# Kernel optimization log

Measured on AMD Instinct MI355X. Metric: run time of the kernel, lower is better.

Reference implementation:

```python
import jax, jax.numpy as jnp
import numpy as np
import math

B, T, M, C, H = 2, 2048, 1024, 512, 8
D = C // H  # head dim = 64


def setup_inputs() -> dict:
    key = jax.random.key(0)
    ks = jax.random.split(key, 6)
    return {
        "x": jax.random.normal(ks[0], (B, T, C), jnp.float32),
        "y": jax.random.normal(ks[1], (B, M, C), jnp.float32),
        "attn_x_mask": jnp.ones((1, 1, T, T), jnp.int32),
        "qkv_w": jax.random.normal(ks[2], (3 * C, C), jnp.float32) * 0.02,
        "qkv_b": jax.random.normal(ks[3], (3 * C,), jnp.float32) * 0.02,
        "proj_w": jax.random.normal(ks[4], (C, C), jnp.float32) * 0.02,
        "proj_b": jax.random.normal(ks[5], (C,), jnp.float32) * 0.02,
    }


def _split_heads(t, n, d):
    # [B, N, C] -> [B, H, N, D]
    b = t.shape[0]
    return t.reshape(b, n, H, d).transpose(0, 2, 1, 3)


def reference(x, y, attn_x_mask, qkv_w, qkv_b, proj_w, proj_b):
    b, t, c = x.shape
    m = y.shape[1]
    d = c // H
    scale = 1.0 / math.sqrt(d)

    # shared qkv projection applied to x and y (torch Linear: x @ W.T + b)
    qkv_x = x @ qkv_w.T + qkv_b
    q_x, k_x, v_x = jnp.split(qkv_x, 3, axis=-1)
    qkv_y = y @ qkv_w.T + qkv_b
    q_y, k_y, v_y = jnp.split(qkv_y, 3, axis=-1)

    q_x, k_x, v_x = (_split_heads(a, t, d) for a in (q_x, k_x, v_x))
    q_y, k_y, v_y = (_split_heads(a, m, d) for a in (q_y, k_y, v_y))

    # x -> y cross attention scores (pre-softmax, reused for chaining)
    catt_x2y = jnp.einsum("bhtd,bhmd->bhtm", q_x, k_y) * scale  # [B,H,T,M]
    cval_x2y = jnp.einsum("bhtm,bhmd->bhtd", jax.nn.softmax(catt_x2y, axis=-1), v_y)
    cval_x2y = cval_x2y.transpose(0, 2, 1, 3).reshape(b, t, c)

    # y -> x scores, then chained through raw x2y scores
    catt_y2x = jnp.einsum("bhmd,bhsd->bhms", q_y, k_x) * scale  # [B,H,M,T]
    chained = jnp.einsum("bhtm,bhms->bhts", catt_x2y, catt_y2x) * scale  # [B,H,T,T]
    chained = jnp.where(attn_x_mask == 0, -jnp.inf, chained)
    cval_y2x = jnp.einsum("bhts,bhsd->bhtd", jax.nn.softmax(chained, axis=-1), v_x)
    cval_y2x = cval_y2x.transpose(0, 2, 1, 3).reshape(b, t, c)

    out = cval_x2y - cval_y2x
    out = out @ proj_w.T + proj_b  # dropout layers are identity in eval mode
    return out
```

## Files before the change

kernel.cpp:

```cpp
#include <hip/hip_runtime.h>


typedef _Float16 half_t;
typedef _Float16 half8 __attribute__((ext_vector_type(8)));
typedef _Float16 half4v __attribute__((ext_vector_type(4)));
typedef float floatx4 __attribute__((ext_vector_type(4)));
typedef int int4v __attribute__((ext_vector_type(4)));

constexpr int Bc = 2, Tc = 2048, Mc = 1024, Cc = 512, Hc = 8, Dc = 64;
constexpr long BTC = (long)Bc * Tc * Cc;
constexpr long ZT  = (long)Bc * Hc * Tc;
constexpr float S1 = 0.18033688f;

enum { EPI_F16STORE = 0, EPI_QKV_XY = 1, EPI_PROJ = 2 };

struct EpiParams {
  half_t* h0;
  half_t* h1;
  half_t* h2;
  half_t* h3;
  half_t* h4;
  half_t* h5;
  half_t* h6;
  float* f0;
  const float* bias;
  float scale;
  int ldc;
  long bstride;
};

__device__ __forceinline__ void gld_lds16(const half_t* g, half_t* l) {
  __builtin_amdgcn_global_load_lds(
      (const __attribute__((address_space(1))) void*)g,
      (__attribute__((address_space(3))) void*)l, 16, 0, 0);
}

__device__ __forceinline__ int pkrtz(float a, float b) {
  return __builtin_bit_cast(int, __builtin_amdgcn_cvt_pkrtz(a, b));
}
__device__ __forceinline__ void pl16(int& a, int& b) {
  asm volatile("v_permlane16_swap_b32 %0, %1" : "+v"(a), "+v"(b));
}
__device__ __forceinline__ void pl32(int& a, int& b) {
  asm volatile("v_permlane32_swap_b32 %0, %1" : "+v"(a), "+v"(b));
}

template <int BM, int BN, int WMG, int WNG, int EPI, int GX = 0, int GY = 0>
__global__ __launch_bounds__(256) void gemm_nt(
    const half_t* __restrict__ A, const half_t* __restrict__ Bt,
    int K, int lda, int ldb, long bsA, long bsB, EpiParams ep)
{
  constexpr int BK = 64;
  constexpr int WTM = BM / WMG, WTN = BN / WNG;
  constexpr int MI = WTM / 16, NI = WTN / 16;
  constexpr int AIT = BM * BK / 8 / 256;
  constexpr int BIT = BN * BK / 8 / 256;
  constexpr int NLD = AIT + BIT;
  __shared__ __align__(16) half_t As[2][BM * BK];
  __shared__ __align__(16) half_t Bs[2][BN * BK];

  const int tid = threadIdx.x;
  const int lane = tid & 63;
  const int wave = tid >> 6;
  const int wm = wave / WNG, wn = wave % WNG;
  const int r16 = lane & 15, g = lane >> 4;
  const int z = blockIdx.z;

  int bxl = blockIdx.x, byl = blockIdx.y;
  if constexpr (GX > 0) {
    constexpr int CHUNK = GX * GY / 8;
    const int f = byl * GX + bxl;
    const int L = (f & 7) * CHUNK + (f >> 3);
    bxl = L % GX; byl = L / GX;
  }
  const long m0 = (long)byl * BM;
  const long n0 = (long)bxl * BN;
  const half_t* Abase = A + (long)z * bsA + m0 * (long)lda;
  const half_t* Bbase = Bt + (long)z * bsB + n0 * (long)ldb;

  const int rA = wm * WTM + r16;
  const int rB = wn * WTN + r16;

  floatx4 acc[MI][NI];
#pragma unroll
  for (int mi = 0; mi < MI; ++mi)
#pragma unroll
    for (int ni = 0; ni < NI; ++ni)
      acc[mi][ni] = floatx4{0.f, 0.f, 0.f, 0.f};

  auto stage = [&](int kt, int buf) {
#pragma unroll
    for (int i = 0; i < AIT; ++i) {
      const int c = tid + i * 256;
      const int row = c >> 3, js = c & 7;
      const int jg = js ^ (row & 7);
      gld_lds16(Abase + (long)row * lda + kt + jg * 8, &As[buf][c * 8]);
    }
#pragma unroll
    for (int i = 0; i < BIT; ++i) {
      const int c = tid + i * 256;
      const int row = c >> 3, js = c & 7;
      const int jg = js ^ (row & 7);
      gld_lds16(Bbase + (long)row * ldb + kt + jg * 8, &Bs[buf][c * 8]);
    }
  };

  const int NIT = K / BK;
  stage(0, 0);
  asm volatile("" ::: "memory");

  for (int it = 0; it < NIT; ++it) {
    const bool hn = (it + 1 < NIT);
    if (hn) stage((it + 1) * BK, (it + 1) & 1);
    asm volatile("" ::: "memory");
    if (hn) {
      if constexpr (NLD == 6) asm volatile("s_waitcnt vmcnt(6)" ::: "memory");
      else if constexpr (NLD == 4) asm volatile("s_waitcnt vmcnt(4)" ::: "memory");
      else if constexpr (NLD == 8) asm volatile("s_waitcnt vmcnt(8)" ::: "memory");
      else asm volatile("s_waitcnt vmcnt(0)" ::: "memory");
    } else {
      asm volatile("s_waitcnt vmcnt(0)" ::: "memory");
    }
    __builtin_amdgcn_s_barrier();
    asm volatile("" ::: "memory");

    const half_t* Ab = As[it & 1];
    const half_t* Bb = Bs[it & 1];
    half8 aF[MI][2], bF[NI][2];
#pragma unroll
    for (int mi = 0; mi < MI; ++mi)
#pragma unroll
      for (int k2 = 0; k2 < 2; ++k2)
        aF[mi][k2] = *reinterpret_cast<const half8*>(
            &Ab[(rA + mi * 16) * BK + ((k2 * 4 + g) ^ (r16 & 7)) * 8]);
#pragma unroll
    for (int ni = 0; ni < NI; ++ni)
#pragma unroll
      for (int k2 = 0; k2 < 2; ++k2)
        bF[ni][k2] = *reinterpret_cast<const half8*>(
            &Bb[(rB + ni * 16) * BK + ((k2 * 4 + g) ^ (r16 & 7)) * 8]);
    __builtin_amdgcn_s_setprio(1);
#pragma unroll
    for (int k2 = 0; k2 < 2; ++k2)
#pragma unroll
      for (int mi = 0; mi < MI; ++mi)
#pragma unroll
        for (int ni = 0; ni < NI; ++ni)
          acc[mi][ni] = __builtin_amdgcn_mfma_f32_16x16x32_f16(
              aF[mi][k2], bF[ni][k2], acc[mi][ni], 0, 0, 0);
    __builtin_amdgcn_s_setprio(0);
    asm volatile("s_waitcnt lgkmcnt(0)" ::: "memory");
    __builtin_amdgcn_s_barrier();
    asm volatile("" ::: "memory");
  }

  half_t* Txp = &As[0][0];
  const bool isx  = (m0 < (long)Bc * Tc);
  const int which = (int)(n0 >> 9);
  const int hh    = ((int)n0 & 511) >> 6;

#pragma unroll
  for (int mi = 0; mi < MI; ++mi) {
#pragma unroll
    for (int ni = 0; ni < NI; ++ni) {
#pragma unroll
      for (int reg = 0; reg < 4; ++reg) {
        const int r = (int)m0 + wm * WTM + mi * 16 + g * 4 + reg;
        const int c = (int)n0 + wn * WTN + ni * 16 + r16;
        const float v = acc[mi][ni][reg];
        if constexpr (EPI == EPI_F16STORE) {
          ep.h0[(long)z * ep.bstride + (long)r * ep.ldc + c] = (half_t)(v * ep.scale);
        } else if constexpr (EPI == EPI_QKV_XY) {
          const float val = v + ep.bias[c];
          const int d = c & 63;
          const int rloc = r - (int)m0;
          if (isx) {
            const int b = (int)(m0 >> 11);
            const int t = r & (Tc - 1);
            const long bh = (long)(b * Hc + hh);
            if (which == 0)      ep.h0[(bh * Tc + t) * Dc + d] = (half_t)(val * S1);
            else if (which == 1) ep.h1[(bh * Tc + t) * Dc + d] = (half_t)val;
            else                 Txp[d * 136 + rloc] = (half_t)val;
          } else {
            const long m2 = m0 - (long)Bc * Tc;
            const int b = (int)(m2 >> 10);
            const int t = (r - Bc * Tc) & (Mc - 1);
            const long bh = (long)(b * Hc + hh);
            if (which == 0)      Txp[d * 136 + rloc] = (half_t)(val * 0.125f);
            else if (which == 1) { ep.h4[(bh * Mc + t) * Dc + d] = (half_t)val;
                                   Txp[d * 136 + rloc] = (half_t)val; }
            else                 Txp[d * 136 + rloc] = (half_t)val;
          }
        } else {
          ep.f0[(long)r * Cc + c] = v + ep.bias[c];
        }
      }
    }
  }

  if constexpr (EPI == EPI_QKV_XY && BM == 128) {
    const bool hasT = isx ? (which == 2) : true;
    if (hasT) {
      __syncthreads();
      half_t* dstT; int L; long tb; int b;
      if (isx) { dstT = ep.h2; L = Tc; tb = m0 & (Tc - 1); b = (int)(m0 >> 11); }
      else {
        const long m2 = m0 - (long)Bc * Tc;
        b = (int)(m2 >> 10); tb = m2 & (Mc - 1); L = Mc;
        dstT = (which == 0) ? ep.h3 : (which == 1) ? ep.h5 : ep.h6;
      }
      const long bh = (long)(b * Hc + hh);
      const int dr = tid >> 2, qd = tid & 3;
      half_t* gbase = dstT + (bh * 64 + dr) * L + tb + qd * 32;
#pragma unroll
      for (int j = 0; j < 4; ++j) {
        const half8 v8 = *reinterpret_cast<const half8*>(&Txp[dr * 136 + qd * 32 + j * 8]);
        *reinterpret_cast<half8*>(&gbase[j * 8]) = v8;
      }
    }
  }
}

__global__ __launch_bounds__(256) void wtq2(
    const half_t* __restrict__ QYT, const half_t* __restrict__ KYT,
    const half_t* __restrict__ QX, half_t* __restrict__ Q2)
{
  __shared__ __align__(16) half_t As[2][4096];
  __shared__ __align__(16) half_t Bs[2][4096];
  __shared__ __align__(16) half_t WTs[4096];
  const int tid = threadIdx.x, lane = tid & 63, wave = tid >> 6;
  const int wm = wave >> 1, wn = wave & 1;
  const int r16 = lane & 15, g = lane >> 4;
  const int f = blockIdx.x;
  const int L = (f & 7) * 32 + (f >> 3);
  const int z = L >> 4;
  const int t0 = (L & 15) * 128;
  const half_t* Aq = QYT + (long)z * Dc * Mc;
  const half_t* Bk = KYT + (long)z * Dc * Mc;

  auto stage1 = [&](int kt, int buf) {
#pragma unroll
    for (int i = 0; i < 2; ++i) {
      const int c = tid + i * 256;
      const int row = c >> 3, js = c & 7, jg = js ^ (row & 7);
      gld_lds16(Aq + (long)row * Mc + kt + jg * 8, &As[buf][c * 8]);
    }
#pragma unroll
    for (int i = 0; i < 2; ++i) {
      const int c = tid + i * 256;
      const int row = c >> 3, js = c & 7, jg = js ^ (row & 7);
      gld_lds16(Bk + (long)row * Mc + kt + jg * 8, &Bs[buf][c * 8]);
    }
  };

  floatx4 acc[2][2];
#pragma unroll
  for (int mi = 0; mi < 2; ++mi)
#pragma unroll
    for (int ni = 0; ni < 2; ++ni) acc[mi][ni] = floatx4{0.f, 0.f, 0.f, 0.f};

  const int rA = wm * 32 + r16, rB = wn * 32 + r16;
  stage1(0, 0);
  asm volatile("" ::: "memory");
  for (int it = 0; it < 16; ++it) {
    const bool hn = (it < 15);
    if (hn) stage1((it + 1) * 64, (it + 1) & 1);
    asm volatile("" ::: "memory");
    if (hn) asm volatile("s_waitcnt vmcnt(4)" ::: "memory");
    else    asm volatile("s_waitcnt vmcnt(0)" ::: "memory");
    __builtin_amdgcn_s_barrier();
    asm volatile("" ::: "memory");
    const half_t* Ab = As[it & 1];
    const half_t* Bb = Bs[it & 1];
    half8 aF[2][2], bF[2][2];
#pragma unroll
    for (int mi = 0; mi < 2; ++mi)
#pragma unroll
      for (int k2 = 0; k2 < 2; ++k2)
        aF[mi][k2] = *reinterpret_cast<const half8*>(
            &Ab[(rA + mi * 16) * 64 + ((k2 * 4 + g) ^ (r16 & 7)) * 8]);
#pragma unroll
    for (int ni = 0; ni < 2; ++ni)
#pragma unroll
      for (int k2 = 0; k2 < 2; ++k2)
        bF[ni][k2] = *reinterpret_cast<const half8*>(
            &Bb[(rB + ni * 16) * 64 + ((k2 * 4 + g) ^ (r16 & 7)) * 8]);
    __builtin_amdgcn_s_setprio(1);
#pragma unroll
    for (int k2 = 0; k2 < 2; ++k2)
#pragma unroll
      for (int mi = 0; mi < 2; ++mi)
#pragma unroll
        for (int ni = 0; ni < 2; ++ni)
          acc[mi][ni] = __builtin_amdgcn_mfma_f32_16x16x32_f16(
              aF[mi][k2], bF[ni][k2], acc[mi][ni], 0, 0, 0);
    __builtin_amdgcn_s_setprio(0);
    asm volatile("s_waitcnt lgkmcnt(0)" ::: "memory");
    __builtin_amdgcn_s_barrier();
    asm volatile("" ::: "memory");
  }

  half_t* P2 = &As[0][0];
#pragma unroll
  for (int i = 0; i < 4; ++i) {
    const int c = tid + i * 256;
    const int row = c >> 3, js = c & 7, jg = js ^ (row & 7);
    gld_lds16(QX + ((long)z * Tc + t0 + row) * 64 + jg * 8, P2 + c * 8);
  }
#pragma unroll
  for (int mi = 0; mi < 2; ++mi)
#pragma unroll
    for (int ni = 0; ni < 2; ++ni)
#pragma unroll
      for (int reg = 0; reg < 4; ++reg) {
        const int r = wm * 32 + mi * 16 + g * 4 + reg;
        const int c = wn * 32 + ni * 16 + r16;
        WTs[r * 64 + (((c >> 3) ^ (r & 7)) << 3) + (c & 7)] =
            (half_t)(acc[mi][ni][reg] * 0.125f);
      }
  __syncthreads();

  floatx4 a2[2][4];
#pragma unroll
  for (int mi = 0; mi < 2; ++mi)
#pragma unroll
    for (int ni = 0; ni < 4; ++ni) a2[mi][ni] = floatx4{0.f, 0.f, 0.f, 0.f};
  const int rA2 = wave * 32 + r16;
  half8 aF2[2][2], bF2[4][2];
#pragma unroll
  for (int mi = 0; mi < 2; ++mi)
#pragma unroll
    for (int k2 = 0; k2 < 2; ++k2)
      aF2[mi][k2] = *reinterpret_cast<const half8*>(
          &P2[(rA2 + mi * 16) * 64 + ((k2 * 4 + g) ^ (r16 & 7)) * 8]);
#pragma unroll
  for (int ni = 0; ni < 4; ++ni)
#pragma unroll
    for (int k2 = 0; k2 < 2; ++k2)
      bF2[ni][k2] = *reinterpret_cast<const half8*>(
          &WTs[(ni * 16 + r16) * 64 + ((k2 * 4 + g) ^ (r16 & 7)) * 8]);
#pragma unroll
  for (int k2 = 0; k2 < 2; ++k2)
#pragma unroll
    for (int mi = 0; mi < 2; ++mi)
#pragma unroll
      for (int ni = 0; ni < 4; ++ni)
        a2[mi][ni] = __builtin_amdgcn_mfma_f32_16x16x32_f16(
            aF2[mi][k2], bF2[ni][k2], a2[mi][ni], 0, 0, 0);
#pragma unroll
  for (int mi = 0; mi < 2; ++mi)
#pragma unroll
    for (int ni = 0; ni < 4; ++ni)
#pragma unroll
      for (int reg = 0; reg < 4; ++reg) {
        const int t = t0 + wave * 32 + mi * 16 + g * 4 + reg;
        const int c = ni * 16 + r16;
        Q2[((long)z * Tc + t) * 64 + c] = (half_t)a2[mi][ni][reg];
      }
}

__device__ __forceinline__ void stageK128(const half_t* Kz, int s0, half_t* dst, int tid) {
#pragma unroll
  for (int i = 0; i < 4; ++i) {
    const int c = tid + i * 256;
    const int row = c >> 3, js = c & 7;
    const int jg = js ^ (row & 7);
    gld_lds16(Kz + (long)(s0 + row) * 64 + jg * 8, dst + c * 8);
  }
}
__device__ __forceinline__ void stageV128(const half_t* Vz, int s0, int Slen, half_t* dst, int tid) {
#pragma unroll
  for (int i = 0; i < 4; ++i) {
    const int c = tid + i * 256;
    const int row = c >> 4, js = c & 15;
    const int jg = js ^ (row & 15);
    gld_lds16(Vz + (long)row * Slen + s0 + jg * 8, dst + c * 8);
  }
}

template <bool MASKED, bool PARTIAL>
__device__ __forceinline__ void flash_body(
    const half_t* __restrict__ Qp, const half_t* __restrict__ Kp,
    const half_t* __restrict__ Vp, const unsigned char* __restrict__ mpk,
    half_t* __restrict__ POh, float* __restrict__ Lp, half_t* __restrict__ outF,
    int Slen, int sbeg, int scount, int z, int q0,
    half_t* Kb0, half_t* Kb1, half_t* Vb)
{
  const int tid = threadIdx.x, lane = tid & 63, w = tid >> 6;
  const int r16 = lane & 15, g = lane >> 4;
  const int b = z >> 3, h = z & 7;
  const int NT = Slen >> 7;
  const half_t* Qz = Qp + ((long)z * Tc + q0) * 64;
  const half_t* Kz = Kp + (long)z * Slen * 64;
  const half_t* Vz = Vp + (long)z * 64 * Slen;

  stageK128(Kz, sbeg, Kb0, tid);
  asm volatile("" ::: "memory");
  stageV128(Vz, sbeg, Slen, Vb, tid);
  asm volatile("" ::: "memory");

  half8 aQ[2][2];
#pragma unroll
  for (int mi = 0; mi < 2; ++mi)
#pragma unroll
    for (int k2 = 0; k2 < 2; ++k2)
      aQ[mi][k2] = *reinterpret_cast<const half8*>(
          Qz + (w * 32 + mi * 16 + r16) * 64 + k2 * 32 + g * 8);

  half8 vones;
#pragma unroll
  for (int j = 0; j < 8; ++j) vones[j] = (half_t)1.f;

  floatx4 oaccT[2][4];
  floatx4 lacc4[2];
#pragma unroll
  for (int mi = 0; mi < 2; ++mi) {
    lacc4[mi] = floatx4{0.f, 0.f, 0.f, 0.f};
#pragma unroll
    for (int no = 0; no < 4; ++no) oaccT[mi][no] = floatx4{0.f, 0.f, 0.f, 0.f};
  }

  const int send = sbeg + scount;
  int cur = 0;
  for (int s0 = sbeg; s0 < send; s0 += 128) {
    const bool hn = (s0 + 128 < send);
    asm volatile("s_waitcnt vmcnt(4)" ::: "memory");
    __builtin_amdgcn_s_barrier();
    asm volatile("" ::: "memory");

    unsigned int mb32[2];
    if constexpr (MASKED) {
      const int tile = s0 >> 7;
#pragma unroll
      for (int mi = 0; mi < 2; ++mi) {
        const int q = q0 + w * 32 + mi * 16 + r16;
        mb32[mi] = *reinterpret_cast<const unsigned int*>(
            mpk + ((long)q * NT + tile) * 16 + 4 * g);
      }
    }

    floatx4 sacc[2][8];
#pragma unroll
    for (int mi = 0; mi < 2; ++mi)
#pragma unroll
      for (int ni = 0; ni < 8; ++ni) sacc[mi][ni] = floatx4{0.f, 0.f, 0.f, 0.f};
    const half_t* Kc = cur ? Kb1 : Kb0;
    __builtin_amdgcn_s_setprio(1);
#pragma unroll
    for (int ni = 0; ni < 8; ++ni) {
      const int rB = ni * 16 + r16;
      const half8 b0 = *reinterpret_cast<const half8*>(&Kc[rB * 64 + (g ^ (rB & 7)) * 8]);
      const half8 b1 = *reinterpret_cast<const half8*>(&Kc[rB * 64 + ((4 + g) ^ (rB & 7)) * 8]);
#pragma unroll
      for (int mi = 0; mi < 2; ++mi) {
        sacc[mi][ni] = __builtin_amdgcn_mfma_f32_16x16x32_f16(b0, aQ[mi][0], sacc[mi][ni], 0, 0, 0);
        sacc[mi][ni] = __builtin_amdgcn_mfma_f32_16x16x32_f16(b1, aQ[mi][1], sacc[mi][ni], 0, 0, 0);
      }
    }
    __builtin_amdgcn_s_setprio(0);
    if (hn) stageK128(Kz, s0 + 128, cur ? Kb0 : Kb1, tid);
    asm volatile("" ::: "memory");

#pragma unroll
    for (int mi = 0; mi < 2; ++mi) {
      if constexpr (MASKED) {
        if (mb32[mi] != 0xffffffffu) {
#pragma unroll
          for (int reg = 0; reg < 4; ++reg)
#pragma unroll
            for (int ni = 0; ni < 8; ++ni)
              if (!((mb32[mi] >> (reg * 8 + ni)) & 1)) sacc[mi][ni][reg] = -__builtin_inff();
        }
      }
#pragma unroll
      for (int ni = 0; ni < 8; ++ni)
#pragma unroll
        for (int reg = 0; reg < 4; ++reg)
          sacc[mi][ni][reg] = __builtin_amdgcn_exp2f(sacc[mi][ni][reg]);
    }

    if (hn) { asm volatile("s_waitcnt vmcnt(4)" ::: "memory"); }
    else    { asm volatile("s_waitcnt vmcnt(0)" ::: "memory"); }
    __builtin_amdgcn_s_barrier();
    asm volatile("" ::: "memory");

#pragma unroll
    for (int c = 0; c < 4; ++c) {
      half8 bVv[4];
#pragma unroll
      for (int no = 0; no < 4; ++no) {
        const int rV = no * 16 + r16;
        bVv[no] = *reinterpret_cast<const half8*>(
            &Vb[rV * 128 + ((c * 4 + g) ^ (rV & 15)) * 8]);
      }
#pragma unroll
      for (int mi = 0; mi < 2; ++mi) {
        int x0 = pkrtz(sacc[mi][2 * c][0],     sacc[mi][2 * c][1]);
        int x1 = pkrtz(sacc[mi][2 * c][2],     sacc[mi][2 * c][3]);
        int x2 = pkrtz(sacc[mi][2 * c + 1][0], sacc[mi][2 * c + 1][1]);
        int x3 = pkrtz(sacc[mi][2 * c + 1][2], sacc[mi][2 * c + 1][3]);
        pl32(x0, x2); pl32(x1, x3);
        pl16(x0, x2); pl16(x1, x3);
        int4v wv; wv[0] = x0; wv[1] = x1; wv[2] = x2; wv[3] = x3;
        const half8 aP = __builtin_bit_cast(half8, wv);
        __builtin_amdgcn_s_setprio(1);
#pragma unroll
        for (int no = 0; no < 4; ++no)
          oaccT[mi][no] = __builtin_amdgcn_mfma_f32_16x16x32_f16(bVv[no], aP, oaccT[mi][no], 0, 0, 0);
        lacc4[mi] = __builtin_amdgcn_mfma_f32_16x16x32_f16(vones, aP, lacc4[mi], 0, 0, 0);
        __builtin_amdgcn_s_setprio(0);
      }
    }
    __builtin_amdgcn_s_barrier();
    asm volatile("" ::: "memory");
    if (hn) stageV128(Vz, s0 + 128, Slen, Vb, tid);
    asm volatile("" ::: "memory");
    cur ^= 1;
  }

  float ls2[2];
#pragma unroll
  for (int mi = 0; mi < 2; ++mi) ls2[mi] = lacc4[mi][0];

  float* slab = reinterpret_cast<float*>(Vb) + w * 1024;
#pragma unroll
  for (int mi = 0; mi < 2; ++mi) {
    const int tq = q0 + w * 32 + mi * 16;
    if constexpr (PARTIAL) {
      if (lane < 16) Lp[(long)z * Tc + tq + r16] = ls2[mi];
    }
    const float sc = PARTIAL ? 1.f : (1.f / ls2[mi]);
#pragma unroll
    for (int no = 0; no < 4; ++no) {
      floatx4 v = oaccT[mi][no];
      if constexpr (!PARTIAL) v *= sc;
      *reinterpret_cast<floatx4*>(&slab[r16 * 64 + no * 16 + (g ^ (r16 & 3)) * 4]) = v;
    }
#pragma unroll
    for (int it = 0; it < 4; ++it) {
      const int q2 = it * 4 + g;
      const int d4 = r16;
      const floatx4 v = *reinterpret_cast<const floatx4*>(
          &slab[q2 * 64 + (d4 >> 2) * 16 + ((d4 & 3) ^ (q2 & 3)) * 4]);
      const long off = ((long)(b * Tc + tq + q2)) * Cc + h * 64 + d4 * 4;
      half4v hh; hh[0] = (half_t)v[0]; hh[1] = (half_t)v[1];
      hh[2] = (half_t)v[2]; hh[3] = (half_t)v[3];
      if constexpr (PARTIAL) {
        *reinterpret_cast<half4v*>(&POh[off]) = hh;
      } else {
        *reinterpret_cast<half4v*>(&outF[off]) = hh;
      }
    }
  }
}

__global__ __launch_bounds__(256, 3) void flash_both(
    const half_t* __restrict__ Q2, const half_t* __restrict__ KX,
    const half_t* __restrict__ VXT, const unsigned char* __restrict__ mpk,
    const half_t* __restrict__ QX, const half_t* __restrict__ KY,
    const half_t* __restrict__ VYT,
    half_t* __restrict__ POh, float* __restrict__ Lp, half_t* __restrict__ DH2)
{
  __shared__ __align__(16) half_t Kb0[8192];
  __shared__ __align__(16) half_t Kb1[8192];
  __shared__ __align__(16) half_t Vb[8192];
  const int bx = blockIdx.x;
  if (bx < 512) {
    const int z  = ((bx & 7) << 1) | ((bx >> 3) & 1);
    const int sh = (bx >> 4) & 1;
    const int q0 = (bx >> 5) * 128;
    flash_body<true, true>(Q2, KX, VXT, mpk,
                           POh + (long)sh * BTC, Lp + (long)sh * ZT, nullptr,
                           Tc, sh * 1024, 1024, z, q0, Kb0, Kb1, Vb);
  } else {
    const int b2 = bx - 512;
    const int z  = ((b2 & 7) << 1) | ((b2 >> 3) & 1);
    const int q0 = (b2 >> 4) * 128;
    flash_body<false, false>(QX, KY, VYT, nullptr,
                             nullptr, nullptr, DH2,
                             Mc, 0, Mc, z, q0, Kb0, Kb1, Vb);
  }
}

__global__ __launch_bounds__(256) void combine_k(
    const half_t* __restrict__ POh, const float* __restrict__ Lp,
    const half_t* __restrict__ DH2, half_t* __restrict__ DH)
{
  const long idx = (long)blockIdx.x * 256 + threadIdx.x;
  const long c4 = idx * 4;
  const int c = (int)(c4 & (Cc - 1));
  const long bt = c4 >> 9;
  const int h = c >> 6;
  const int b = (int)(bt >> 11), t = (int)(bt & (Tc - 1));
  const long zt = (long)(b * Hc + h) * Tc + t;
  const float ainv = 1.f / (Lp[zt] + Lp[ZT + zt]);
  const half4v oa0 = reinterpret_cast<const half4v*>(POh)[idx];
  const half4v oa1 = reinterpret_cast<const half4v*>(POh)[BTC / 4 + idx];
  const half4v dv = reinterpret_cast<const half4v*>(DH2)[idx];
  half4v r;
  r[0] = (half_t)((float)dv[0] - ((float)oa0[0] + (float)oa1[0]) * ainv);
  r[1] = (half_t)((float)dv[1] - ((float)oa0[1] + (float)oa1[1]) * ainv);
  r[2] = (half_t)((float)dv[2] - ((float)oa0[2] + (float)oa1[2]) * ainv);
  r[3] = (half_t)((float)dv[3] - ((float)oa0[3] + (float)oa1[3]) * ainv);
  reinterpret_cast<half4v*>(DH)[idx] = r;
}

__device__ __forceinline__ void cvt4(const float* in, half_t* out, long i) {
  const float4 f = reinterpret_cast<const float4*>(in)[i];
  half4v h; h[0] = (half_t)f.x; h[1] = (half_t)f.y; h[2] = (half_t)f.z; h[3] = (half_t)f.w;
  reinterpret_cast<half4v*>(out)[i] = h;
}

__global__ __launch_bounds__(256) void prep(
    const float* __restrict__ x, const float* __restrict__ y,
    const float* __restrict__ qw, const float* __restrict__ pw,
    const int* __restrict__ mask,
    half_t* __restrict__ XH, half_t* __restrict__ YH,
    half_t* __restrict__ WQ, half_t* __restrict__ WP,
    unsigned char* __restrict__ mpk)
{
  const long i = (long)blockIdx.x * 256 + threadIdx.x;
  constexpr long n0 = 524288;
  constexpr long n1 = n0 + 262144;
  constexpr long n2 = n1 + 196608;
  constexpr long n3 = n2 + 65536;
  if (i < n0) cvt4(x, XH, i);
  else if (i < n1) cvt4(y, YH, i - n0);
  else if (i < n2) cvt4(qw, WQ, i - n1);
  else if (i < n3) cvt4(pw, WP, i - n2);
  else {
    const long idx = i - n3;
    const int t = (int)(idx >> 8), tile = (int)((idx >> 4) & 15), r16 = (int)(idx & 15);
    const int* row = mask + (long)t * Tc + tile * 128 + r16;
    unsigned int bbits = 0;
#pragma unroll
    for (int ni = 0; ni < 8; ++ni)
      bbits |= (row[ni * 16] != 0 ? 1u : 0u) << ni;
    mpk[idx] = (unsigned char)bbits;
  }
}

constexpr size_t OFF_XH   = 0;
constexpr size_t OFF_YH   = OFF_XH   + (size_t)Bc*Tc*Cc*2;
constexpr size_t OFF_WQ   = OFF_YH   + (size_t)Bc*Mc*Cc*2;
constexpr size_t OFF_WP   = OFF_WQ   + (size_t)3*Cc*Cc*2;
constexpr size_t OFF_QX   = OFF_WP   + (size_t)Cc*Cc*2;
constexpr size_t OFF_KX   = OFF_QX   + (size_t)Bc*Hc*Tc*Dc*2;
constexpr size_t OFF_VXT  = OFF_KX   + (size_t)Bc*Hc*Tc*Dc*2;
constexpr size_t OFF_QYT  = OFF_VXT  + (size_t)Bc*Hc*Tc*Dc*2;
constexpr size_t OFF_KY   = OFF_QYT  + (size_t)Bc*Hc*Mc*Dc*2;
constexpr size_t OFF_KYT  = OFF_KY   + (size_t)Bc*Hc*Mc*Dc*2;
constexpr size_t OFF_VYT  = OFF_KYT  + (size_t)Bc*Hc*Mc*Dc*2;
constexpr size_t OFF_Q2   = OFF_VYT  + (size_t)Bc*Hc*Mc*Dc*2;
constexpr size_t OFF_DH   = OFF_Q2   + (size_t)Bc*Hc*Tc*Dc*2;
constexpr size_t OFF_DH2  = OFF_DH   + (size_t)Bc*Tc*Cc*2;
constexpr size_t OFF_MPK  = OFF_DH2  + (size_t)Bc*Tc*Cc*2;
constexpr size_t OFF_PO   = OFF_MPK  + (size_t)Tc*256;
constexpr size_t OFF_L    = OFF_PO   + (size_t)2*BTC*2;

extern "C" void kernel_launch(void* const* d_in, const int* in_sizes, int n_in,
                              void* d_out, int out_size, void* d_ws, size_t ws_size,
                              hipStream_t stream) {
  const float* x      = (const float*)d_in[0];
  const float* y      = (const float*)d_in[1];
  const int*   mask   = (const int*)  d_in[2];
  const float* qkv_b  = (const float*)d_in[4];
  const float* proj_b = (const float*)d_in[6];
  float* out = (float*)d_out;
  char* ws = (char*)d_ws;

  half_t* XH   = (half_t*)(ws + OFF_XH);
  half_t* YH   = (half_t*)(ws + OFF_YH);
  half_t* WQ   = (half_t*)(ws + OFF_WQ);
  half_t* WP   = (half_t*)(ws + OFF_WP);
  half_t* QX   = (half_t*)(ws + OFF_QX);
  half_t* KX   = (half_t*)(ws + OFF_KX);
  half_t* VXT  = (half_t*)(ws + OFF_VXT);
  half_t* QYT  = (half_t*)(ws + OFF_QYT);
  half_t* KY   = (half_t*)(ws + OFF_KY);
  half_t* KYT  = (half_t*)(ws + OFF_KYT);
  half_t* VYT  = (half_t*)(ws + OFF_VYT);
  half_t* Q2   = (half_t*)(ws + OFF_Q2);
  half_t* DH   = (half_t*)(ws + OFF_DH);
  half_t* DH2  = (half_t*)(ws + OFF_DH2);
  unsigned char* MPK = (unsigned char*)(ws + OFF_MPK);
  half_t* POh  = (half_t*)(ws + OFF_PO);
  float*  Lp   = (float*) (ws + OFF_L);

  prep<<<6144, 256, 0, stream>>>(x, y, (const float*)d_in[3], (const float*)d_in[5],
                                 mask, XH, YH, WQ, WP, MPK);

  {
    EpiParams ep{};
    ep.h0 = QX; ep.h1 = KX; ep.h2 = VXT; ep.h3 = QYT;
    ep.h4 = KY; ep.h5 = KYT; ep.h6 = VYT; ep.bias = qkv_b;
    gemm_nt<128,64,2,2,EPI_QKV_XY,24,48><<<dim3(24, 48, 1), 256, 0, stream>>>(
        XH, WQ, Cc, Cc, Cc, 0, 0, ep);
  }

  wtq2<<<dim3(256), 256, 0, stream>>>(QYT, KYT, QX, Q2);

  flash_both<<<dim3(768), 256, 0, stream>>>(
      Q2, KX, VXT, MPK, QX, KY, VYT, POh, Lp, DH2);

  combine_k<<<(int)(BTC/4/256), 256, 0, stream>>>(POh, Lp, DH2, DH);

  {
    EpiParams ep{}; ep.f0 = out; ep.bias = proj_b;
    gemm_nt<64,64,2,2,EPI_PROJ,8,64><<<dim3(8, 64, 1), 256, 0, stream>>>(
        DH, WP, Cc, Cc, Cc, 0, 0, ep);
  }
}
```

Baseline: 173.5 us.

## Split flash attention into finer KV chunks with 64-wide tiles and six-way combine

```diff
diff --git a/kernel.cpp b/kernel.cpp
--- a/kernel.cpp
+++ b/kernel.cpp
@@ -359,32 +359,31 @@
       }
 }
 
-__device__ __forceinline__ void stageK128(const half_t* Kz, int s0, half_t* dst, int tid) {
-#pragma unroll
-  for (int i = 0; i < 4; ++i) {
+__device__ __forceinline__ void stageK64(const half_t* Kz, int s0, half_t* dst, int tid) {
+#pragma unroll
+  for (int i = 0; i < 2; ++i) {
     const int c = tid + i * 256;
     const int row = c >> 3, js = c & 7;
     const int jg = js ^ (row & 7);
     gld_lds16(Kz + (long)(s0 + row) * 64 + jg * 8, dst + c * 8);
   }
 }
-__device__ __forceinline__ void stageV128(const half_t* Vz, int s0, int Slen, half_t* dst, int tid) {
-#pragma unroll
-  for (int i = 0; i < 4; ++i) {
+__device__ __forceinline__ void stageV64(const half_t* Vz, int s0, int Slen, half_t* dst, int tid) {
+#pragma unroll
+  for (int i = 0; i < 2; ++i) {
     const int c = tid + i * 256;
-    const int row = c >> 4, js = c & 15;
-    const int jg = js ^ (row & 15);
+    const int row = c >> 3, js = c & 7;
+    const int jg = js ^ (row & 7);
     gld_lds16(Vz + (long)row * Slen + s0 + jg * 8, dst + c * 8);
   }
 }
 
-template <bool MASKED, bool PARTIAL>
+template <bool MASKED>
 __device__ __forceinline__ void flash_body(
     const half_t* __restrict__ Qp, const half_t* __restrict__ Kp,
     const half_t* __restrict__ Vp, const unsigned char* __restrict__ mpk,
-    half_t* __restrict__ POh, float* __restrict__ Lp, half_t* __restrict__ outF,
-    int Slen, int sbeg, int scount, int z, int q0,
-    half_t* Kb0, half_t* Kb1, half_t* Vb)
+    half_t* __restrict__ POh, float* __restrict__ Lp,
+    int Slen, int sbeg, int z, int q0, half_t* lds)
 {
   const int tid = threadIdx.x, lane = tid & 63, w = tid >> 6;
   const int r16 = lane & 15, g = lane >> 4;
@@ -393,10 +392,13 @@
   const half_t* Qz = Qp + ((long)z * Tc + q0) * 64;
   const half_t* Kz = Kp + (long)z * Slen * 64;
   const half_t* Vz = Vp + (long)z * 64 * Slen;
-
-  stageK128(Kz, sbeg, Kb0, tid);
+  half_t* Kb0 = lds;
+  half_t* Kb1 = lds + 4096;
+  half_t* Vb  = lds + 8192;
+
+  stageK64(Kz, sbeg, Kb0, tid);
   asm volatile("" ::: "memory");
-  stageV128(Vz, sbeg, Slen, Vb, tid);
+  stageV64(Vz, sbeg, Slen, Vb, tid);
   asm volatile("" ::: "memory");
 
   half8 aQ[2][2];
@@ -420,11 +422,11 @@
     for (int no = 0; no < 4; ++no) oaccT[mi][no] = floatx4{0.f, 0.f, 0.f, 0.f};
   }
 
-  const int send = sbeg + scount;
+  const int send = sbeg + 512;
   int cur = 0;
-  for (int s0 = sbeg; s0 < send; s0 += 128) {
-    const bool hn = (s0 + 128 < send);
-    asm volatile("s_waitcnt vmcnt(4)" ::: "memory");
+  for (int s0 = sbeg; s0 < send; s0 += 64) {
+    const bool hn = (s0 + 64 < send);
+    asm volatile("s_waitcnt vmcnt(2)" ::: "memory");
     __builtin_amdgcn_s_barrier();
     asm volatile("" ::: "memory");
 
@@ -438,16 +440,18 @@
             mpk + ((long)q * NT + tile) * 16 + 4 * g);
       }
     }
-
-    floatx4 sacc[2][8];
+    const int hf4 = ((s0 >> 6) & 1) ? 4 : 0;
+    const unsigned int fullm = hf4 ? 0xf0f0f0f0u : 0x0f0f0f0fu;
+
+    floatx4 sacc[2][4];
 #pragma unroll
     for (int mi = 0; mi < 2; ++mi)
 #pragma unroll
-      for (int ni = 0; ni < 8; ++ni) sacc[mi][ni] = floatx4{0.f, 0.f, 0.f, 0.f};
+      for (int ni = 0; ni < 4; ++ni) sacc[mi][ni] = floatx4{0.f, 0.f, 0.f, 0.f};
     const half_t* Kc = cur ? Kb1 : Kb0;
     __builtin_amdgcn_s_setprio(1);
 #pragma unroll
-    for (int ni = 0; ni < 8; ++ni) {
+    for (int ni = 0; ni < 4; ++ni) {
       const int rB = ni * 16 + r16;
       const half8 b0 = *reinterpret_cast<const half8*>(&Kc[rB * 64 + (g ^ (rB & 7)) * 8]);
       const half8 b1 = *reinterpret_cast<const half8*>(&Kc[rB * 64 + ((4 + g) ^ (rB & 7)) * 8]);
@@ -458,40 +462,40 @@
       }
     }
     __builtin_amdgcn_s_setprio(0);
-    if (hn) stageK128(Kz, s0 + 128, cur ? Kb0 : Kb1, tid);
+    if (hn) stageK64(Kz, s0 + 64, cur ? Kb0 : Kb1, tid);
     asm volatile("" ::: "memory");
 
 #pragma unroll
     for (int mi = 0; mi < 2; ++mi) {
       if constexpr (MASKED) {
-        if (mb32[mi] != 0xffffffffu) {
+        if ((mb32[mi] & fullm) != fullm) {
 #pragma unroll
           for (int reg = 0; reg < 4; ++reg)
 #pragma unroll
-            for (int ni = 0; ni < 8; ++ni)
-              if (!((mb32[mi] >> (reg * 8 + ni)) & 1)) sacc[mi][ni][reg] = -__builtin_inff();
+            for (int ni = 0; ni < 4; ++ni)
+              if (!((mb32[mi] >> (reg * 8 + ni + hf4)) & 1)) sacc[mi][ni][reg] = -__builtin_inff();
         }
       }
 #pragma unroll
-      for (int ni = 0; ni < 8; ++ni)
+      for (int ni = 0; ni < 4; ++ni)
 #pragma unroll
         for (int reg = 0; reg < 4; ++reg)
           sacc[mi][ni][reg] = __builtin_amdgcn_exp2f(sacc[mi][ni][reg]);
     }
 
-    if (hn) { asm volatile("s_waitcnt vmcnt(4)" ::: "memory"); }
+    if (hn) { asm volatile("s_waitcnt vmcnt(2)" ::: "memory"); }
     else    { asm volatile("s_waitcnt vmcnt(0)" ::: "memory"); }
     __builtin_amdgcn_s_barrier();
     asm volatile("" ::: "memory");
 
 #pragma unroll
-    for (int c = 0; c < 4; ++c) {
+    for (int c = 0; c < 2; ++c) {
       half8 bVv[4];
 #pragma unroll
       for (int no = 0; no < 4; ++no) {
         const int rV = no * 16 + r16;
         bVv[no] = *reinterpret_cast<const half8*>(
-            &Vb[rV * 128 + ((c * 4 + g) ^ (rV & 15)) * 8]);
+            &Vb[rV * 64 + ((c * 4 + g) ^ (rV & 7)) * 8]);
       }
 #pragma unroll
       for (int mi = 0; mi < 2; ++mi) {
@@ -513,7 +517,7 @@
     }
     __builtin_amdgcn_s_barrier();
     asm volatile("" ::: "memory");
-    if (hn) stageV128(Vz, s0 + 128, Slen, Vb, tid);
+    if (hn) stageV64(Vz, s0 + 64, Slen, Vb, tid);
     asm volatile("" ::: "memory");
     cur ^= 1;
   }
@@ -522,18 +526,14 @@
 #pragma unroll
   for (int mi = 0; mi < 2; ++mi) ls2[mi] = lacc4[mi][0];
 
-  float* slab = reinterpret_cast<float*>(Vb) + w * 1024;
+  float* slab = reinterpret_cast<float*>(lds) + w * 1024;
 #pragma unroll
   for (int mi = 0; mi < 2; ++mi) {
     const int tq = q0 + w * 32 + mi * 16;
-    if constexpr (PARTIAL) {
-      if (lane < 16) Lp[(long)z * Tc + tq + r16] = ls2[mi];
-    }
-    const float sc = PARTIAL ? 1.f : (1.f / ls2[mi]);
+    if (lane < 16) Lp[(long)z * Tc + tq + r16] = ls2[mi];
 #pragma unroll
     for (int no = 0; no < 4; ++no) {
       floatx4 v = oaccT[mi][no];
-      if constexpr (!PARTIAL) v *= sc;
       *reinterpret_cast<floatx4*>(&slab[r16 * 64 + no * 16 + (g ^ (r16 & 3)) * 4]) = v;
     }
 #pragma unroll
@@ -545,46 +545,41 @@
       const long off = ((long)(b * Tc + tq + q2)) * Cc + h * 64 + d4 * 4;
       half4v hh; hh[0] = (half_t)v[0]; hh[1] = (half_t)v[1];
       hh[2] = (half_t)v[2]; hh[3] = (half_t)v[3];
-      if constexpr (PARTIAL) {
-        *reinterpret_cast<half4v*>(&POh[off]) = hh;
-      } else {
-        *reinterpret_cast<half4v*>(&outF[off]) = hh;
-      }
-    }
-  }
-}
-
-__global__ __launch_bounds__(256, 3) void flash_both(
+      *reinterpret_cast<half4v*>(&POh[off]) = hh;
+    }
+  }
+}
+
+__global__ __launch_bounds__(256, 4) void flash_both(
     const half_t* __restrict__ Q2, const half_t* __restrict__ KX,
     const half_t* __restrict__ VXT, const unsigned char* __restrict__ mpk,
     const half_t* __restrict__ QX, const half_t* __restrict__ KY,
     const half_t* __restrict__ VYT,
-    half_t* __restrict__ POh, float* __restrict__ Lp, half_t* __restrict__ DH2)
+    half_t* __restrict__ POh, float* __restrict__ Lp)
 {
-  __shared__ __align__(16) half_t Kb0[8192];
-  __shared__ __align__(16) half_t Kb1[8192];
-  __shared__ __align__(16) half_t Vb[8192];
+  __shared__ __align__(16) half_t lds[12288];
   const int bx = blockIdx.x;
-  if (bx < 512) {
+  if (bx < 1024) {
     const int z  = ((bx & 7) << 1) | ((bx >> 3) & 1);
-    const int sh = (bx >> 4) & 1;
-    const int q0 = (bx >> 5) * 128;
-    flash_body<true, true>(Q2, KX, VXT, mpk,
-                           POh + (long)sh * BTC, Lp + (long)sh * ZT, nullptr,
-                           Tc, sh * 1024, 1024, z, q0, Kb0, Kb1, Vb);
+    const int qt = (bx >> 4) & 3;
+    const int q0 = (bx >> 6) * 128;
+    flash_body<true>(Q2, KX, VXT, mpk,
+                     POh + (long)qt * BTC, Lp + (long)qt * ZT,
+                     Tc, qt * 512, z, q0, lds);
   } else {
-    const int b2 = bx - 512;
+    const int b2 = bx - 1024;
     const int z  = ((b2 & 7) << 1) | ((b2 >> 3) & 1);
-    const int q0 = (b2 >> 4) * 128;
-    flash_body<false, false>(QX, KY, VYT, nullptr,
-                             nullptr, nullptr, DH2,
-                             Mc, 0, Mc, z, q0, Kb0, Kb1, Vb);
+    const int sh = (b2 >> 4) & 1;
+    const int q0 = (b2 >> 5) * 128;
+    flash_body<false>(QX, KY, VYT, nullptr,
+                      POh + (long)(4 + sh) * BTC, Lp + (long)(4 + sh) * ZT,
+                      Mc, sh * 512, z, q0, lds);
   }
 }
 
 __global__ __launch_bounds__(256) void combine_k(
     const half_t* __restrict__ POh, const float* __restrict__ Lp,
-    const half_t* __restrict__ DH2, half_t* __restrict__ DH)
+    half_t* __restrict__ DH)
 {
   const long idx = (long)blockIdx.x * 256 + threadIdx.x;
   const long c4 = idx * 4;
@@ -593,15 +588,24 @@
   const int h = c >> 6;
   const int b = (int)(bt >> 11), t = (int)(bt & (Tc - 1));
   const long zt = (long)(b * Hc + h) * Tc + t;
-  const float ainv = 1.f / (Lp[zt] + Lp[ZT + zt]);
-  const half4v oa0 = reinterpret_cast<const half4v*>(POh)[idx];
-  const half4v oa1 = reinterpret_cast<const half4v*>(POh)[BTC / 4 + idx];
-  const half4v dv = reinterpret_cast<const half4v*>(DH2)[idx];
+  const float i0 = 1.f / (Lp[zt] + Lp[ZT + zt] + Lp[2 * ZT + zt] + Lp[3 * ZT + zt]);
+  const float i1 = 1.f / (Lp[4 * ZT + zt] + Lp[5 * ZT + zt]);
+  float a0[4] = {0.f, 0.f, 0.f, 0.f}, a1[4] = {0.f, 0.f, 0.f, 0.f};
+#pragma unroll
+  for (int s = 0; s < 4; ++s) {
+    const half4v o = reinterpret_cast<const half4v*>(POh)[s * (BTC / 4) + idx];
+#pragma unroll
+    for (int j = 0; j < 4; ++j) a0[j] += (float)o[j];
+  }
+#pragma unroll
+  for (int s = 4; s < 6; ++s) {
+    const half4v o = reinterpret_cast<const half4v*>(POh)[s * (BTC / 4) + idx];
+#pragma unroll
+    for (int j = 0; j < 4; ++j) a1[j] += (float)o[j];
+  }
   half4v r;
-  r[0] = (half_t)((float)dv[0] - ((float)oa0[0] + (float)oa1[0]) * ainv);
-  r[1] = (half_t)((float)dv[1] - ((float)oa0[1] + (float)oa1[1]) * ainv);
-  r[2] = (half_t)((float)dv[2] - ((float)oa0[2] + (float)oa1[2]) * ainv);
-  r[3] = (half_t)((float)dv[3] - ((float)oa0[3] + (float)oa1[3]) * ainv);
+#pragma unroll
+  for (int j = 0; j < 4; ++j) r[j] = (half_t)(a1[j] * i1 - a0[j] * i0);
   reinterpret_cast<half4v*>(DH)[idx] = r;
 }
 
@@ -653,10 +657,9 @@
 constexpr size_t OFF_VYT  = OFF_KYT  + (size_t)Bc*Hc*Mc*Dc*2;
 constexpr size_t OFF_Q2   = OFF_VYT  + (size_t)Bc*Hc*Mc*Dc*2;
 constexpr size_t OFF_DH   = OFF_Q2   + (size_t)Bc*Hc*Tc*Dc*2;
-constexpr size_t OFF_DH2  = OFF_DH   + (size_t)Bc*Tc*Cc*2;
-constexpr size_t OFF_MPK  = OFF_DH2  + (size_t)Bc*Tc*Cc*2;
+constexpr size_t OFF_MPK  = OFF_DH   + (size_t)Bc*Tc*Cc*2;
 constexpr size_t OFF_PO   = OFF_MPK  + (size_t)Tc*256;
-constexpr size_t OFF_L    = OFF_PO   + (size_t)2*BTC*2;
+constexpr size_t OFF_L    = OFF_PO   + (size_t)6*BTC*2;
 
 extern "C" void kernel_launch(void* const* d_in, const int* in_sizes, int n_in,
                               void* d_out, int out_size, void* d_ws, size_t ws_size,
@@ -682,7 +685,6 @@
   half_t* VYT  = (half_t*)(ws + OFF_VYT);
   half_t* Q2   = (half_t*)(ws + OFF_Q2);
   half_t* DH   = (half_t*)(ws + OFF_DH);
-  half_t* DH2  = (half_t*)(ws + OFF_DH2);
   unsigned char* MPK = (unsigned char*)(ws + OFF_MPK);
   half_t* POh  = (half_t*)(ws + OFF_PO);
   float*  Lp   = (float*) (ws + OFF_L);
@@ -700,10 +702,10 @@
 
   wtq2<<<dim3(256), 256, 0, stream>>>(QYT, KYT, QX, Q2);
 
-  flash_both<<<dim3(768), 256, 0, stream>>>(
-      Q2, KX, VXT, MPK, QX, KY, VYT, POh, Lp, DH2);
-
-  combine_k<<<(int)(BTC/4/256), 256, 0, stream>>>(POh, Lp, DH2, DH);
+  flash_both<<<dim3(1536), 256, 0, stream>>>(
+      Q2, KX, VXT, MPK, QX, KY, VYT, POh, Lp);
+
+  combine_k<<<(int)(BTC/4/256), 256, 0, stream>>>(POh, Lp, DH);
 
   {
     EpiParams ep{}; ep.f0 = out; ep.bias = proj_b;
```

After: 171.5 us. No clear change (-1.2%).
